# Optimization experiments

Measured on AMD Instinct MI355X. Metric: run time of the kernel, lower is better.

## Reference

```python
import jax, jax.numpy as jnp
import numpy as np
from jax.scipy.linalg import expm

B, T = 32, 4096
FREQ_DIM = 128
HID = 64
OUT_DIM = 2
N_COMP = 4
DT = 0.1
EPS = 1e-5


def setup_inputs() -> dict:
    key = jax.random.key(0)
    ks = jax.random.split(key, 16)
    f32 = jnp.float32

    def lin(k, out_d, in_d):
        bound = 1.0 / np.sqrt(in_d)
        kw, kb = jax.random.split(k)
        W = jax.random.uniform(kw, (out_d, in_d), f32, -bound, bound)
        b = jax.random.uniform(kb, (out_d,), f32, -bound, bound)
        return W, b

    x = jax.random.normal(ks[0], (B, T, 1), f32)
    # EnhancedWavePhysics params
    freq_spectrum = jnp.linspace(1.0, 20.0, FREQ_DIM, dtype=f32)
    pm_w1, pm_b1 = lin(ks[1], 128, 1)
    pm_w2, pm_b2 = lin(ks[2], FREQ_DIM * 2, 128)
    wc_w, wc_b = lin(ks[3], HID, FREQ_DIM)
    amp_ctrl = jnp.ones((1,), f32) * 0.1
    # quantum encoder
    qe_w1, qe_b1 = lin(ks[4], HID * 2, HID)
    qe_w2, qe_b2 = lin(ks[5], HID * 4, HID * 2)
    # layernorm
    ln_g = jnp.ones((HID * 4,), f32)
    ln_b = jnp.zeros((HID * 4,), f32)
    # skew-symmetric hamiltonians [4, 64, 64]
    A = jax.random.normal(ks[6], (N_COMP, HID, HID), f32) * 0.05
    hams = (A - jnp.swapaxes(A, -1, -2)) / 2.0
    # interference net
    int_w1, int_b1 = lin(ks[7], 32, 4)
    int_w2, int_b2 = lin(ks[8], OUT_DIM, 32)
    int_strength = jnp.ones((1,), f32)
    return dict(x=x, freq_spectrum=freq_spectrum, pm_w1=pm_w1, pm_b1=pm_b1,
                pm_w2=pm_w2, pm_b2=pm_b2, wc_w=wc_w, wc_b=wc_b,
                amp_ctrl=amp_ctrl, qe_w1=qe_w1, qe_b1=qe_b1, qe_w2=qe_w2,
                qe_b2=qe_b2, ln_g=ln_g, ln_b=ln_b, hams=hams,
                int_w1=int_w1, int_b1=int_b1, int_w2=int_w2, int_b2=int_b2,
                int_strength=int_strength)


def reference(x, freq_spectrum, pm_w1, pm_b1, pm_w2, pm_b2, wc_w, wc_b,
              amp_ctrl, qe_w1, qe_b1, qe_w2, qe_b2, ln_g, ln_b, hams,
              int_w1, int_b1, int_w2, int_b2, int_strength):
    Bx, Tx, _ = x.shape
    # --- EnhancedWavePhysics ---
    mod = jnp.tanh(x @ pm_w1.T + pm_b1) @ pm_w2.T + pm_b2            # [B,T,2F]
    amplitude, phase = jnp.split(mod, 2, axis=-1)                     # [B,T,F]
    amplitude = jnp.tanh(amplitude) * amp_ctrl
    time = jnp.linspace(0.0, 2.0 * np.pi, Tx)[None, :, None]          # [1,T,1]
    freqs = freq_spectrum[None, None, :]                              # [1,1,F]
    wave_components = amplitude * jnp.sin(freqs * time + phase)       # [B,T,F]
    wave_field = jnp.tanh(wave_components @ wc_w.T + wc_b)            # [B,T,H]
    # --- quantum encoder + layernorm ---
    q = jnp.tanh(wave_field @ qe_w1.T + qe_b1) @ qe_w2.T + qe_b2      # [B,T,4H]
    mu = q.mean(-1, keepdims=True)
    var = q.var(-1, keepdims=True)
    q = (q - mu) / jnp.sqrt(var + EPS) * ln_g + ln_b
    psi = q.reshape(Bx, Tx, N_COMP, HID)                              # [B,T,C,D]
    # --- Hamiltonian evolution: torch does matrix_exp(-1j*(1j*H)*dt)=expm(H*dt)
    #     (H skew-symmetric real => U real orthogonal), then psi @ U.T, take real.
    U = jax.vmap(expm)(hams * DT)                                     # [C,D,D]
    evolved = jnp.einsum('btcd,ced->btce', psi, U)                    # [B,T,C,D]
    # --- EnhancedInterference ---
    spec = jnp.abs(jnp.fft.fft(evolved, axis=1))                      # [B,T,C,D]
    freq_w = jax.nn.softmax(spec.mean(-1), axis=1)                    # [B,T,C]
    weighted = jnp.sum(spec * freq_w[..., None], axis=1)              # [B,C,D]
    spatial_avg = weighted.mean(-1)                                   # [B,C]
    out = jnp.tanh(spatial_avg @ int_w1.T + int_b1) @ int_w2.T + int_b2
    return out * int_strength                                         # [B,out_dim]
```

## Files before the change

kernel.cpp:

```cpp
#include <hip/hip_runtime.h>
#include <hip/hip_bf16.h>

#define TT 4096
#define BB 32

typedef unsigned short ushort_t;
typedef __attribute__((ext_vector_type(8))) short short8v;
typedef __attribute__((ext_vector_type(4))) float float4v;

__device__ inline ushort_t bf16rn(float v) {
    unsigned u = __float_as_uint(v);
    unsigned r = (u + 0x7FFFu + ((u >> 16) & 1u)) >> 16;
    return (ushort_t)r;
}
__device__ inline float bf16tof(ushort_t h) {
    return __uint_as_float(((unsigned)h) << 16);
}
__device__ inline int SW(int i) { return i + (i >> 5); }

__device__ inline float fast_tanh(float x) {
    float e = __builtin_amdgcn_exp2f(x * 2.8853900817779268f);
    return 1.0f - 2.0f * __builtin_amdgcn_rcpf(e + 1.0f);
}
__device__ inline float fast_sin(float x) {
    return __builtin_amdgcn_sinf(x * 0.15915494309189535f);
}

__global__ __launch_bounds__(256) void k1_expm(const float* __restrict__ hams,
                                               ushort_t* __restrict__ Uhi,
                                               ushort_t* __restrict__ Ulo)
{
    int c = blockIdx.x, tid = threadIdx.x;
    __shared__ float M[4096], P[4096], Acc[4096];
    const float* H = hams + c * 4096;
    for (int k = tid; k < 4096; k += 256) {
        float m = H[k] * 0.1f;
        M[k] = m; P[k] = m;
        Acc[k] = m + (((k >> 6) == (k & 63)) ? 1.0f : 0.0f);
    }
    __syncthreads();
    int j = tid & 63;
    float mcol[64];
    #pragma unroll
    for (int k = 0; k < 64; k++) mcol[k] = M[k * 64 + j];
    for (int term = 2; term <= 8; term++) {
        float inv = 1.0f / (float)term;
        float np_[16];
        #pragma unroll
        for (int r = 0; r < 16; r++) {
            int i = (tid >> 6) + 4 * r;
            float a = 0.f;
            #pragma unroll
            for (int k = 0; k < 64; k++) a = fmaf(P[i * 64 + k], mcol[k], a);
            np_[r] = a * inv;
        }
        __syncthreads();
        #pragma unroll
        for (int r = 0; r < 16; r++) {
            int i = (tid >> 6) + 4 * r;
            P[i * 64 + j] = np_[r];
            Acc[i * 64 + j] += np_[r];
        }
        __syncthreads();
    }
    for (int k = tid; k < 4096; k += 256) {
        float v = Acc[k];
        ushort_t h = bf16rn(v);
        Uhi[c * 4096 + k] = h;
        Ulo[c * 4096 + k] = bf16rn(v - bf16tof(h));
    }
}

__global__ void split_all(const float* __restrict__ pw2, const float* __restrict__ wcw,
                          const float* __restrict__ qw1, const float* __restrict__ qw2,
                          ushort_t* __restrict__ wb)
{
    int i = blockIdx.x * 256 + threadIdx.x;
    const float* src; ushort_t *hi, *lo; int off;
    if (i < 32768)      { src = pw2; hi = wb;          lo = wb + 32768;  off = i; }
    else if (i < 40960) { src = wcw; hi = wb + 65536;  lo = wb + 73728;  off = i - 32768; }
    else if (i < 49152) { src = qw1; hi = wb + 81920;  lo = wb + 90112;  off = i - 40960; }
    else                { src = qw2; hi = wb + 98304;  lo = wb + 131072; off = i - 49152; }
    float v = src[off];
    ushort_t h = bf16rn(v);
    hi[off] = h;
    lo[off] = bf16rn(v - bf16tof(h));
}

__global__ __launch_bounds__(256, 2) void gemm_s1(
    const ushort_t* __restrict__ Whi, const ushort_t* __restrict__ Wlo,
    const float* __restrict__ bias,
    const float* __restrict__ x, const float* __restrict__ pw1,
    const float* __restrict__ pb1,
    const float* __restrict__ freq, const float* __restrict__ ampc,
    ushort_t* __restrict__ O)
{
    __shared__ ushort_t OT[2][2048];
    int tid = threadIdx.x;
    int w = tid >> 6, l = tid & 63, l15 = l & 15, kg = l >> 4;
    int kofb = kg * 8;

    short8v bh[4][4], bl[4][4];
    #pragma unroll
    for (int i = 0; i < 4; i++) {
        int n = (w + 4 * i) * 16 + l15;
        #pragma unroll
        for (int kc = 0; kc < 4; kc++) {
            int kof = kc * 32 + kofb;
            bh[i][kc] = *(const short8v*)(Whi + (size_t)n * 128 + kof);
            bl[i][kc] = *(const short8v*)(Wlo + (size_t)n * 128 + kof);
        }
    }
    float am = ampc[0];
    float fr[2], ba[2], bp[2];
    #pragma unroll
    for (int i = 0; i < 2; i++) {
        int f = (w + 4 * i) * 16 + l15;
        fr[i] = freq[f]; ba[i] = bias[f]; bp[i] = bias[128 + f];
    }

    int mbase = blockIdx.x * 64;
    for (int mi = 0; mi < 4; mi++) {
        int m0 = mbase + mi * 16;
        float xv = x[m0 + l15];
        short8v ah[4], al[4];
        #pragma unroll
        for (int kc = 0; kc < 4; kc++) {
            int k0 = kc * 32 + kofb;
            float4 w0 = *(const float4*)(pw1 + k0);
            float4 w1v = *(const float4*)(pw1 + k0 + 4);
            float4 b0 = *(const float4*)(pb1 + k0);
            float4 b1v = *(const float4*)(pb1 + k0 + 4);
            #pragma unroll
            for (int j = 0; j < 8; j++) {
                float wj = (j < 4) ? (&w0.x)[j] : (&w1v.x)[j - 4];
                float bj = (j < 4) ? (&b0.x)[j] : (&b1v.x)[j - 4];
                float v = fast_tanh(fmaf(xv, wj, bj));
                ushort_t h = bf16rn(v);
                ah[kc][j] = (short)h;
                al[kc][j] = (short)bf16rn(v - bf16tof(h));
            }
        }
        float4v acc[4];
        #pragma unroll
        for (int i = 0; i < 4; i++) acc[i] = (float4v){0.f, 0.f, 0.f, 0.f};
        #pragma unroll
        for (int kc = 0; kc < 4; kc++) {
            #pragma unroll
            for (int i = 0; i < 4; i++) {
                acc[i] = __builtin_amdgcn_mfma_f32_16x16x32_bf16(ah[kc], bh[i][kc], acc[i], 0, 0, 0);
                acc[i] = __builtin_amdgcn_mfma_f32_16x16x32_bf16(ah[kc], bl[i][kc], acc[i], 0, 0, 0);
                acc[i] = __builtin_amdgcn_mfma_f32_16x16x32_bf16(al[kc], bh[i][kc], acc[i], 0, 0, 0);
            }
        }
        int buf = mi & 1;
        #pragma unroll
        for (int i = 0; i < 2; i++) {
            int f = (w + 4 * i) * 16 + l15;
            #pragma unroll
            for (int r = 0; r < 4; r++) {
                int m = m0 + kg * 4 + r;
                float timev = 6.283185307179586f * (float)(m & 4095) / 4095.0f;
                float a = fast_tanh(acc[i][r] + ba[i]) * am;
                float ph = acc[i + 2][r] + bp[i];
                float v = a * fast_sin(fmaf(fr[i], timev, ph));
                OT[buf][(kg * 4 + r) * 128 + f] = bf16rn(v);
            }
        }
        __syncthreads();
        *(uint4*)(O + (size_t)m0 * 128 + tid * 8) = *(const uint4*)(&OT[buf][tid * 8]);
    }
}

__global__ __launch_bounds__(256, 2) void s23_v2(
    const ushort_t* __restrict__ A,
    const ushort_t* __restrict__ W2hi, const ushort_t* __restrict__ W2lo,
    const float* __restrict__ b2,
    const ushort_t* __restrict__ W3hi, const ushort_t* __restrict__ W3lo,
    const float* __restrict__ b3,
    ushort_t* __restrict__ OHi, ushort_t* __restrict__ OLo)
{
    __shared__ unsigned WF[2][16][65];
    __shared__ ushort_t OThi[2][2048], OTlo[2][2048];
    int tid = threadIdx.x;
    int w = tid >> 6, l = tid & 63, l15 = l & 15, kg = l >> 4;
    int kofb = kg * 8;

    short8v w2h[4], w2l[4];
    #pragma unroll
    for (int kc = 0; kc < 4; kc++) {
        int n = w * 16 + l15;
        int kof = kc * 32 + kofb;
        w2h[kc] = *(const short8v*)(W2hi + (size_t)n * 128 + kof);
        w2l[kc] = *(const short8v*)(W2lo + (size_t)n * 128 + kof);
    }
    short8v w3h[2][2], w3l[2][2];
    #pragma unroll
    for (int i = 0; i < 2; i++) {
        int n = (w + 4 * i) * 16 + l15;
        #pragma unroll
        for (int kc = 0; kc < 2; kc++) {
            int kof = kc * 32 + kofb;
            w3h[i][kc] = *(const short8v*)(W3hi + (size_t)n * 64 + kof);
            w3l[i][kc] = *(const short8v*)(W3lo + (size_t)n * 64 + kof);
        }
    }
    float b2v = b2[w * 16 + l15];
    float b3v[2];
    #pragma unroll
    for (int i = 0; i < 2; i++) b3v[i] = b3[(w + 4 * i) * 16 + l15];

    int mbase = blockIdx.x * 64;
    for (int mi = 0; mi < 4; mi++) {
        int m0 = mbase + mi * 16;
        short8v ah[4];
        #pragma unroll
        for (int kc = 0; kc < 4; kc++) {
            int kof = kc * 32 + kofb;
            ah[kc] = *(const short8v*)(A + (size_t)(m0 + l15) * 128 + kof);
        }
        float4v acc1 = (float4v){0.f, 0.f, 0.f, 0.f};
        #pragma unroll
        for (int kc = 0; kc < 4; kc++) {
            acc1 = __builtin_amdgcn_mfma_f32_16x16x32_bf16(ah[kc], w2h[kc], acc1, 0, 0, 0);
            acc1 = __builtin_amdgcn_mfma_f32_16x16x32_bf16(ah[kc], w2l[kc], acc1, 0, 0, 0);
        }
        int buf = mi & 1;
        #pragma unroll
        for (int r = 0; r < 4; r++) {
            float v = fast_tanh(acc1[r] + b2v);
            ushort_t h = bf16rn(v);
            ushort_t lo2 = bf16rn(v - bf16tof(h));
            WF[buf][kg * 4 + r][w * 16 + l15] = (unsigned)h | ((unsigned)lo2 << 16);
        }
        __syncthreads();
        float4v acc2[2];
        acc2[0] = (float4v){0.f, 0.f, 0.f, 0.f};
        acc2[1] = (float4v){0.f, 0.f, 0.f, 0.f};
        #pragma unroll
        for (int kc = 0; kc < 2; kc++) {
            short8v a2h, a2l;
            #pragma unroll
            for (int j = 0; j < 8; j++) {
                unsigned u = WF[buf][l15][kc * 32 + kofb + j];
                a2h[j] = (short)(u & 0xFFFFu);
                a2l[j] = (short)(u >> 16);
            }
            #pragma unroll
            for (int i = 0; i < 2; i++) {
                acc2[i] = __builtin_amdgcn_mfma_f32_16x16x32_bf16(a2h, w3h[i][kc], acc2[i], 0, 0, 0);
                acc2[i] = __builtin_amdgcn_mfma_f32_16x16x32_bf16(a2h, w3l[i][kc], acc2[i], 0, 0, 0);
                acc2[i] = __builtin_amdgcn_mfma_f32_16x16x32_bf16(a2l, w3h[i][kc], acc2[i], 0, 0, 0);
            }
        }
        #pragma unroll
        for (int i = 0; i < 2; i++) {
            int n = (w + 4 * i) * 16 + l15;
            #pragma unroll
            for (int r = 0; r < 4; r++) {
                float v = fast_tanh(acc2[i][r] + b3v[i]);
                ushort_t h = bf16rn(v);
                OThi[buf][(kg * 4 + r) * 128 + n] = h;
                OTlo[buf][(kg * 4 + r) * 128 + n] = bf16rn(v - bf16tof(h));
            }
        }
        __syncthreads();
        *(uint4*)(OHi + (size_t)m0 * 128 + tid * 8) = *(const uint4*)(&OThi[buf][tid * 8]);
        *(uint4*)(OLo + (size_t)m0 * 128 + tid * 8) = *(const uint4*)(&OTlo[buf][tid * 8]);
    }
}

__global__ __launch_bounds__(256, 2) void gemm_s4e(
    const ushort_t* __restrict__ Ahi, const ushort_t* __restrict__ Alo,
    const ushort_t* __restrict__ Whi, const ushort_t* __restrict__ Wlo,
    const float* __restrict__ bias,
    const float* __restrict__ lng, const float* __restrict__ lnb,
    const ushort_t* __restrict__ Uhi, const ushort_t* __restrict__ Ulo,
    unsigned* __restrict__ psiu)
{
    __shared__ float partS[2][4][16], partSS[2][4][16];
    __shared__ unsigned PT[256 * 33];
    int tid = threadIdx.x;
    int w = tid >> 6, l = tid & 63, l15 = l & 15, kg = l >> 4;
    int kofb = kg * 8;

    short8v bh[4][4], bl[4][4];
    #pragma unroll
    for (int i = 0; i < 4; i++) {
        int n = (w + 4 * i) * 16 + l15;
        #pragma unroll
        for (int kc = 0; kc < 4; kc++) {
            int kof = kc * 32 + kofb;
            bh[i][kc] = *(const short8v*)(Whi + (size_t)n * 128 + kof);
            bl[i][kc] = *(const short8v*)(Wlo + (size_t)n * 128 + kof);
        }
    }
    float bv[4], g4[4], be4[4];
    #pragma unroll
    for (int i = 0; i < 4; i++) {
        int n = (w + 4 * i) * 16 + l15;
        bv[i] = bias[n]; g4[i] = lng[n]; be4[i] = lnb[n];
    }

    int mbase = blockIdx.x * 32;
    int b = mbase >> 12, tbase = mbase & 4095;

    short8v a0h[4], a0l[4], a1h[4], a1l[4];
    #pragma unroll
    for (int kc = 0; kc < 4; kc++) {
        int kof = kc * 32 + kofb;
        a0h[kc] = *(const short8v*)(Ahi + (size_t)(mbase + l15) * 128 + kof);
        a0l[kc] = *(const short8v*)(Alo + (size_t)(mbase + l15) * 128 + kof);
        a1h[kc] = *(const short8v*)(Ahi + (size_t)(mbase + 16 + l15) * 128 + kof);
        a1l[kc] = *(const short8v*)(Alo + (size_t)(mbase + 16 + l15) * 128 + kof);
    }

    float4v acc0[4], acc1[4];
    #pragma unroll
    for (int i = 0; i < 4; i++) {
        acc0[i] = (float4v){0.f, 0.f, 0.f, 0.f};
        acc1[i] = (float4v){0.f, 0.f, 0.f, 0.f};
    }
    #pragma unroll
    for (int kc = 0; kc < 4; kc++) {
        #pragma unroll
        for (int i = 0; i < 4; i++) {
            acc0[i] = __builtin_amdgcn_mfma_f32_16x16x32_bf16(a0h[kc], bh[i][kc], acc0[i], 0, 0, 0);
            acc0[i] = __builtin_amdgcn_mfma_f32_16x16x32_bf16(a0h[kc], bl[i][kc], acc0[i], 0, 0, 0);
            acc0[i] = __builtin_amdgcn_mfma_f32_16x16x32_bf16(a0l[kc], bh[i][kc], acc0[i], 0, 0, 0);
        }
    }
    #pragma unroll
    for (int kc = 0; kc < 4; kc++) {
        #pragma unroll
        for (int i = 0; i < 4; i++) {
            acc1[i] = __builtin_amdgcn_mfma_f32_16x16x32_bf16(a1h[kc], bh[i][kc], acc1[i], 0, 0, 0);
            acc1[i] = __builtin_amdgcn_mfma_f32_16x16x32_bf16(a1h[kc], bl[i][kc], acc1[i], 0, 0, 0);
            acc1[i] = __builtin_amdgcn_mfma_f32_16x16x32_bf16(a1l[kc], bh[i][kc], acc1[i], 0, 0, 0);
        }
    }

    #pragma unroll
    for (int mi = 0; mi < 2; mi++) {
        float4v* acc = (mi == 0) ? acc0 : acc1;
        float s[4] = {0, 0, 0, 0}, ss[4] = {0, 0, 0, 0};
        #pragma unroll
        for (int i = 0; i < 4; i++) {
            #pragma unroll
            for (int r = 0; r < 4; r++) {
                float v = acc[i][r] + bv[i];
                s[r] += v; ss[r] += v * v;
            }
        }
        #pragma unroll
        for (int r = 0; r < 4; r++) {
            #pragma unroll
            for (int off = 1; off < 16; off <<= 1) {
                s[r] += __shfl_xor(s[r], off);
                ss[r] += __shfl_xor(ss[r], off);
            }
        }
        if (l15 == 0) {
            #pragma unroll
            for (int r = 0; r < 4; r++) {
                partS[mi][w][kg * 4 + r] = s[r];
                partSS[mi][w][kg * 4 + r] = ss[r];
            }
        }
    }
    __syncthreads();

    #pragma unroll
    for (int mi = 0; mi < 2; mi++) {
        float4v* acc = (mi == 0) ? acc0 : acc1;
        float mu[4], rstd[4];
        #pragma unroll
        for (int r = 0; r < 4; r++) {
            float ts = 0.f, tss = 0.f;
            #pragma unroll
            for (int wv = 0; wv < 4; wv++) {
                ts += partS[mi][wv][kg * 4 + r];
                tss += partSS[mi][wv][kg * 4 + r];
            }
            mu[r] = ts * (1.0f / 256.0f);
            float var = tss * (1.0f / 256.0f) - mu[r] * mu[r];
            rstd[r] = rsqrtf(var + 1e-5f);
        }
        #pragma unroll
        for (int i = 0; i < 4; i++) {
            int n = (w + 4 * i) * 16 + l15;
            #pragma unroll
            for (int r = 0; r < 4; r++) {
                float v = (acc[i][r] + bv[i] - mu[r]) * rstd[r] * g4[i] + be4[i];
                ushort_t h = bf16rn(v);
                ushort_t lo2 = bf16rn(v - bf16tof(h));
                PT[n * 33 + mi * 16 + kg * 4 + r] = (unsigned)h | ((unsigned)lo2 << 16);
            }
        }
    }
    __syncthreads();

    int c = w;
    size_t gb = ((size_t)(b * 256 + c * 64)) * 4096 + tbase;
    #pragma unroll
    for (int et = 0; et < 4; et++) {
        short8v ua_h[2], ua_l[2];
        #pragma unroll
        for (int kc = 0; kc < 2; kc++) {
            size_t uo = (size_t)c * 4096 + (et * 16 + l15) * 64 + kc * 32 + kofb;
            ua_h[kc] = *(const short8v*)(Uhi + uo);
            ua_l[kc] = *(const short8v*)(Ulo + uo);
        }
        #pragma unroll
        for (int tt = 0; tt < 2; tt++) {
            float4v acc = (float4v){0.f, 0.f, 0.f, 0.f};
            #pragma unroll
            for (int kc = 0; kc < 2; kc++) {
                short8v b_h, b_l;
                #pragma unroll
                for (int j = 0; j < 8; j++) {
                    unsigned u = PT[(c * 64 + kc * 32 + kofb + j) * 33 + tt * 16 + l15];
                    b_h[j] = (short)(u & 0xFFFFu);
                    b_l[j] = (short)(u >> 16);
                }
                acc = __builtin_amdgcn_mfma_f32_16x16x32_bf16(ua_h[kc], b_h, acc, 0, 0, 0);
                acc = __builtin_amdgcn_mfma_f32_16x16x32_bf16(ua_h[kc], b_l, acc, 0, 0, 0);
                acc = __builtin_amdgcn_mfma_f32_16x16x32_bf16(ua_l[kc], b_h, acc, 0, 0, 0);
            }
            #pragma unroll
            for (int r = 0; r < 4; r++) {
                int e = et * 16 + kg * 4 + r;
                float v = acc[r];
                ushort_t h = bf16rn(v);
                ushort_t lo2 = bf16rn(v - bf16tof(h));
                psiu[gb + (size_t)e * 4096 + tt * 16 + l15] =
                    (unsigned)h | ((unsigned)lo2 << 16);
            }
        }
    }
}

__global__ __launch_bounds__(256, 2) void k3b_fft(const unsigned* __restrict__ ev,
                                                  float* __restrict__ msum8)
{
    __shared__ float re[4224], im[4224];
    int b = blockIdx.x, c = blockIdx.y, g = blockIdx.z;
    int tid = threadIdx.x;

    float macc[8];
    #pragma unroll
    for (int r = 0; r < 8; r++) macc[r] = 0.f;
    float macc8 = 0.f;

    size_t base = (((size_t)b * 4 + c) * 64 + (size_t)g * 8) * TT;
    for (int p = 0; p < 4; p++) {
        __syncthreads();
        for (int r = 0; r < 4; r++) {
            int t0 = (r * 256 + tid) * 4;
            uint4 va = *(const uint4*)(ev + base + (size_t)(2 * p) * TT + t0);
            uint4 vb = *(const uint4*)(ev + base + (size_t)(2 * p + 1) * TT + t0);
            #pragma unroll
            for (int j = 0; j < 4; j++) {
                int rv = __brev((unsigned)(t0 + j)) >> 20;
                unsigned ua = (&va.x)[j], ub = (&vb.x)[j];
                re[SW(rv)] = bf16tof((ushort_t)(ua & 0xFFFFu)) + bf16tof((ushort_t)(ua >> 16));
                im[SW(rv)] = bf16tof((ushort_t)(ub & 0xFFFFu)) + bf16tof((ushort_t)(ub >> 16));
            }
        }
        __syncthreads();

        #pragma unroll
        for (int trip = 0; trip < 3; trip++) {
            const int sh = trip * 4;
            int pos = tid & ((1 << sh) - 1);
            int grp = tid >> sh;
            int i0 = (grp << (sh + 4)) + pos;

            float yr[16], yi[16];
            #pragma unroll
            for (int j = 0; j < 16; j++) {
                int a = SW(i0 + (j << sh));
                yr[j] = re[a]; yi[j] = im[a];
            }
            float ang = -(float)pos / (float)(16 << sh);
            float t1r = __builtin_amdgcn_cosf(ang);
            float t1i = __builtin_amdgcn_sinf(ang);
            float t2r = t1r * t1r - t1i * t1i, t2i = 2.f * t1r * t1i;
            float t4r = t2r * t2r - t2i * t2i, t4i = 2.f * t2r * t2i;
            float t8r = t4r * t4r - t4i * t4i, t8i = 2.f * t4r * t4i;

            #pragma unroll
            for (int m = 0; m < 8; m++) {
                int j0 = 2 * m, j1 = j0 + 1;
                float tr = t8r * yr[j1] - t8i * yi[j1];
                float ti = t8r * yi[j1] + t8i * yr[j1];
                yr[j1] = yr[j0] - tr; yi[j1] = yi[j0] - ti;
                yr[j0] += tr;         yi[j0] += ti;
            }
            #pragma unroll
            for (int bs = 0; bs < 16; bs += 4) {
                {
                    int j0 = bs, j1 = bs + 2;
                    float tr = t4r * yr[j1] - t4i * yi[j1];
                    float ti = t4r * yi[j1] + t4i * yr[j1];
                    yr[j1] = yr[j0] - tr; yi[j1] = yi[j0] - ti;
                    yr[j0] += tr;         yi[j0] += ti;
                }
                {
                    int j0 = bs + 1, j1 = bs + 3;
                    float tr = t4i * yr[j1] + t4r * yi[j1];
                    float ti = t4i * yi[j1] - t4r * yr[j1];
                    yr[j1] = yr[j0] - tr; yi[j1] = yi[j0] - ti;
                    yr[j0] += tr;         yi[j0] += ti;
                }
            }
            {
                float wr = t2r, wi = t2i;
                #pragma unroll
                for (int j = 0; j < 4; j++) {
                    #pragma unroll
                    for (int bs = 0; bs < 16; bs += 8) {
                        int j0 = bs + j, j1 = j0 + 4;
                        float tr = wr * yr[j1] - wi * yi[j1];
                        float ti = wr * yi[j1] + wi * yr[j1];
                        yr[j1] = yr[j0] - tr; yi[j1] = yi[j0] - ti;
                        yr[j0] += tr;         yi[j0] += ti;
                    }
                    float nwr = (wr + wi) * 0.70710678f;
                    float nwi = (wi - wr) * 0.70710678f;
                    wr = nwr; wi = nwi;
                }
            }
            {
                float wr = t1r, wi = t1i;
                #pragma unroll
                for (int j = 0; j < 8; j++) {
                    int j0 = j, j1 = j + 8;
                    float tr = wr * yr[j1] - wi * yi[j1];
                    float ti = wr * yi[j1] + wi * yr[j1];
                    yr[j1] = yr[j0] - tr; yi[j1] = yi[j0] - ti;
                    yr[j0] += tr;         yi[j0] += ti;
                    float nwr = wr * 0.92387953f + wi * 0.38268343f;
                    float nwi = wi * 0.92387953f - wr * 0.38268343f;
                    wr = nwr; wi = nwi;
                }
            }
            #pragma unroll
            for (int j = 0; j < 16; j++) {
                int a = SW(i0 + (j << sh));
                re[a] = yr[j]; im[a] = yi[j];
            }
            __syncthreads();
        }

        for (int r = 0; r < 8; r++) {
            int k = tid + r * 256;
            int mk = (4096 - k) & 4095;
            float rk = re[SW(k)], ik = im[SW(k)];
            float rm = re[SW(mk)], imm = im[SW(mk)];
            float dA1 = rk + rm, dA2 = ik - imm;
            float dB1 = ik + imm, dB2 = rk - rm;
            float magA = 0.5f * sqrtf(dA1 * dA1 + dA2 * dA2);
            float magB = 0.5f * sqrtf(dB1 * dB1 + dB2 * dB2);
            macc[r] += magA + magB;
        }
        if (tid == 0) {
            float rk = re[SW(2048)], ik = im[SW(2048)];
            macc8 += fabsf(rk) + fabsf(ik);
        }
    }
    float* ms = msum8 + (((size_t)b * 4 + c) * 8 + g) * 4096;
    for (int r = 0; r < 8; r++) {
        int k = tid + r * 256;
        ms[k] = macc[r];
        if (k > 0) ms[4096 - k] = macc[r];
    }
    if (tid == 0) ms[2048] = macc8;
}

__global__ __launch_bounds__(256) void k4_softdot(const float* __restrict__ msum8,
                                                  float* __restrict__ sa)
{
    __shared__ float m[4096];
    __shared__ float red[256];
    int bc = blockIdx.x, tid = threadIdx.x;
    const float* ms = msum8 + (size_t)bc * 8 * 4096;
    float lmax = -1e30f;
    for (int k = tid; k < 4096; k += 256) {
        float v = 0.f;
        #pragma unroll
        for (int g = 0; g < 8; g++) v += ms[g * 4096 + k];
        v *= (1.0f / 64.0f);
        m[k] = v;
        lmax = fmaxf(lmax, v);
    }
    red[tid] = lmax; __syncthreads();
    for (int s2 = 128; s2 > 0; s2 >>= 1) {
        if (tid < s2) red[tid] = fmaxf(red[tid], red[tid + s2]);
        __syncthreads();
    }
    float mx = red[0]; __syncthreads();
    float lsum = 0.f, ldot = 0.f;
    for (int k = tid; k < 4096; k += 256) {
        float e = expf(m[k] - mx);
        lsum += e; ldot += e * m[k];
    }
    red[tid] = lsum; __syncthreads();
    for (int s2 = 128; s2 > 0; s2 >>= 1) {
        if (tid < s2) red[tid] += red[tid + s2];
        __syncthreads();
    }
    float tsum = red[0]; __syncthreads();
    red[tid] = ldot; __syncthreads();
    for (int s2 = 128; s2 > 0; s2 >>= 1) {
        if (tid < s2) red[tid] += red[tid + s2];
        __syncthreads();
    }
    if (tid == 0) sa[bc] = red[0] / tsum;
}

__global__ void k5_head(const float* __restrict__ sa,
                        const float* __restrict__ w1, const float* __restrict__ b1,
                        const float* __restrict__ w2, const float* __restrict__ b2,
                        const float* __restrict__ strength,
                        float* __restrict__ out)
{
    int b = threadIdx.x;
    if (b >= 32) return;
    float s0 = sa[b * 4 + 0], s1 = sa[b * 4 + 1];
    float s2 = sa[b * 4 + 2], s3 = sa[b * 4 + 3];
    float h[32];
    #pragma unroll
    for (int j = 0; j < 32; j++)
        h[j] = tanhf(b1[j] + w1[j * 4 + 0] * s0 + w1[j * 4 + 1] * s1 +
                     w1[j * 4 + 2] * s2 + w1[j * 4 + 3] * s3);
    float st = strength[0];
    #pragma unroll
    for (int o = 0; o < 2; o++) {
        float a = b2[o];
        #pragma unroll
        for (int j = 0; j < 32; j++) a = fmaf(w2[o * 32 + j], h[j], a);
        out[b * 2 + o] = a * st;
    }
}

extern "C" void kernel_launch(void* const* d_in, const int* in_sizes, int n_in,
                              void* d_out, int out_size, void* d_ws, size_t ws_size,
                              hipStream_t stream)
{
    const float* x    = (const float*)d_in[0];
    const float* freq = (const float*)d_in[1];
    const float* pw1  = (const float*)d_in[2];
    const float* pb1  = (const float*)d_in[3];
    const float* pw2  = (const float*)d_in[4];
    const float* pb2  = (const float*)d_in[5];
    const float* wcw  = (const float*)d_in[6];
    const float* wcb  = (const float*)d_in[7];
    const float* ampc = (const float*)d_in[8];
    const float* qw1  = (const float*)d_in[9];
    const float* qb1  = (const float*)d_in[10];
    const float* qw2  = (const float*)d_in[11];
    const float* qb2  = (const float*)d_in[12];
    const float* lng  = (const float*)d_in[13];
    const float* lnb  = (const float*)d_in[14];
    const float* hams = (const float*)d_in[15];
    const float* iw1  = (const float*)d_in[16];
    const float* ib1  = (const float*)d_in[17];
    const float* iw2  = (const float*)d_in[18];
    const float* ib2  = (const float*)d_in[19];
    const float* istr = (const float*)d_in[20];

    char* wsb = (char*)d_ws;
    ushort_t* AHi = (ushort_t*)(wsb + 0);
    ushort_t* ALo = (ushort_t*)(wsb + 33554432);
    ushort_t* Bwcf = (ushort_t*)(wsb + 67108864);
    unsigned* psi = (unsigned*)(wsb + 67108864);
    float*    msum8 = (float*)(wsb + 0);
    ushort_t* Uhi  = (ushort_t*)(wsb + 201326592);
    ushort_t* Ulo  = (ushort_t*)(wsb + 201359360);
    float*    sa   = (float*)(wsb + 201392128);
    ushort_t* wb   = (ushort_t*)(wsb + 203489792);
    ushort_t *pw2hi = wb,          *pw2lo = wb + 32768;
    ushort_t *wcwhi = wb + 65536,  *wcwlo = wb + 73728;
    ushort_t *qw1hi = wb + 81920,  *qw1lo = wb + 90112;
    ushort_t *qw2hi = wb + 98304,  *qw2lo = wb + 131072;
    float* out = (float*)d_out;

    k1_expm<<<4, 256, 0, stream>>>(hams, Uhi, Ulo);
    split_all<<<320, 256, 0, stream>>>(pw2, wcw, qw1, qw2, wb);

    gemm_s1<<<2048, 256, 0, stream>>>(pw2hi, pw2lo, pb2, x, pw1, pb1,
                                      freq, ampc, Bwcf);
    s23_v2<<<2048, 256, 0, stream>>>(Bwcf, wcwhi, wcwlo, wcb,
        qw1hi, qw1lo, qb1, AHi, ALo);
    gemm_s4e<<<4096, 256, 0, stream>>>(AHi, ALo, qw2hi, qw2lo, qb2,
        lng, lnb, Uhi, Ulo, psi);

    k3b_fft<<<dim3(32, 4, 8), 256, 0, stream>>>(psi, msum8);
    k4_softdot<<<128, 256, 0, stream>>>(msum8, sa);
    k5_head<<<1, 64, 0, stream>>>(sa, iw1, ib1, iw2, ib2, istr, out);
}
```

Baseline: 381.8 us.

## Fuse wave-compress, encoder layers and layernorm into one kernel

Merges the s23 kernel (wave-compress GEMM plus first encoder layer) with the second encoder GEMM, layernorm and Hamiltonian kernel into a single kernel. The hi/lo split intermediate no longer goes to global memory and is passed through shared memory instead. The qw2 weight fragments are now loaded from global (cached) memory inside the loop rather than held in registers, which saves registers but adds repeated loads. The FFT magnitude also switches to the hardware sqrt intrinsic.

```diff
diff --git a/kernel.cpp b/kernel.cpp
--- a/kernel.cpp
+++ b/kernel.cpp
@@ -172,16 +172,22 @@
     }
 }
 
-__global__ __launch_bounds__(256, 2) void s23_v2(
+__global__ __launch_bounds__(256, 2) void gemm_s234e(
     const ushort_t* __restrict__ A,
     const ushort_t* __restrict__ W2hi, const ushort_t* __restrict__ W2lo,
     const float* __restrict__ b2,
     const ushort_t* __restrict__ W3hi, const ushort_t* __restrict__ W3lo,
     const float* __restrict__ b3,
-    ushort_t* __restrict__ OHi, ushort_t* __restrict__ OLo)
+    const ushort_t* __restrict__ W4hi, const ushort_t* __restrict__ W4lo,
+    const float* __restrict__ b4,
+    const float* __restrict__ lng, const float* __restrict__ lnb,
+    const ushort_t* __restrict__ Uhi, const ushort_t* __restrict__ Ulo,
+    unsigned* __restrict__ psiu)
 {
     __shared__ unsigned WF[2][16][65];
-    __shared__ ushort_t OThi[2][2048], OTlo[2][2048];
+    __shared__ unsigned Q1[2][16][132];
+    __shared__ float partS[2][4][16], partSS[2][4][16];
+    __shared__ unsigned PT[256 * 33];
     int tid = threadIdx.x;
     int w = tid >> 6, l = tid & 63, l15 = l & 15, kg = l >> 4;
     int kofb = kg * 8;
@@ -209,9 +215,25 @@
     float b3v[2];
     #pragma unroll
     for (int i = 0; i < 2; i++) b3v[i] = b3[(w + 4 * i) * 16 + l15];
-
-    int mbase = blockIdx.x * 64;
-    for (int mi = 0; mi < 4; mi++) {
+    float bv[4], g4[4], be4[4];
+    #pragma unroll
+    for (int i = 0; i < 4; i++) {
+        int n = (w + 4 * i) * 16 + l15;
+        bv[i] = b4[n]; g4[i] = lng[n]; be4[i] = lnb[n];
+    }
+
+    int mbase = blockIdx.x * 32;
+    int b = mbase >> 12, tbase = mbase & 4095;
+
+    float4v acc0[4], acc1[4];
+    #pragma unroll
+    for (int i = 0; i < 4; i++) {
+        acc0[i] = (float4v){0.f, 0.f, 0.f, 0.f};
+        acc1[i] = (float4v){0.f, 0.f, 0.f, 0.f};
+    }
+
+    #pragma unroll
+    for (int mi = 0; mi < 2; mi++) {
         int m0 = mbase + mi * 16;
         short8v ah[4];
         #pragma unroll
@@ -219,38 +241,37 @@
             int kof = kc * 32 + kofb;
             ah[kc] = *(const short8v*)(A + (size_t)(m0 + l15) * 128 + kof);
         }
-        float4v acc1 = (float4v){0.f, 0.f, 0.f, 0.f};
+        float4v acw = (float4v){0.f, 0.f, 0.f, 0.f};
         #pragma unroll
         for (int kc = 0; kc < 4; kc++) {
-            acc1 = __builtin_amdgcn_mfma_f32_16x16x32_bf16(ah[kc], w2h[kc], acc1, 0, 0, 0);
-            acc1 = __builtin_amdgcn_mfma_f32_16x16x32_bf16(ah[kc], w2l[kc], acc1, 0, 0, 0);
-        }
-        int buf = mi & 1;
+            acw = __builtin_amdgcn_mfma_f32_16x16x32_bf16(ah[kc], w2h[kc], acw, 0, 0, 0);
+            acw = __builtin_amdgcn_mfma_f32_16x16x32_bf16(ah[kc], w2l[kc], acw, 0, 0, 0);
+        }
         #pragma unroll
         for (int r = 0; r < 4; r++) {
-            float v = fast_tanh(acc1[r] + b2v);
+            float v = fast_tanh(acw[r] + b2v);
             ushort_t h = bf16rn(v);
             ushort_t lo2 = bf16rn(v - bf16tof(h));
-            WF[buf][kg * 4 + r][w * 16 + l15] = (unsigned)h | ((unsigned)lo2 << 16);
-        }
-        __syncthreads();
-        float4v acc2[2];
-        acc2[0] = (float4v){0.f, 0.f, 0.f, 0.f};
-        acc2[1] = (float4v){0.f, 0.f, 0.f, 0.f};
+            WF[mi][kg * 4 + r][w * 16 + l15] = (unsigned)h | ((unsigned)lo2 << 16);
+        }
+        __syncthreads();
+        float4v acq[2];
+        acq[0] = (float4v){0.f, 0.f, 0.f, 0.f};
+        acq[1] = (float4v){0.f, 0.f, 0.f, 0.f};
         #pragma unroll
         for (int kc = 0; kc < 2; kc++) {
             short8v a2h, a2l;
             #pragma unroll
             for (int j = 0; j < 8; j++) {
-                unsigned u = WF[buf][l15][kc * 32 + kofb + j];
+                unsigned u = WF[mi][l15][kc * 32 + kofb + j];
                 a2h[j] = (short)(u & 0xFFFFu);
                 a2l[j] = (short)(u >> 16);
             }
             #pragma unroll
             for (int i = 0; i < 2; i++) {
-                acc2[i] = __builtin_amdgcn_mfma_f32_16x16x32_bf16(a2h, w3h[i][kc], acc2[i], 0, 0, 0);
-                acc2[i] = __builtin_amdgcn_mfma_f32_16x16x32_bf16(a2h, w3l[i][kc], acc2[i], 0, 0, 0);
-                acc2[i] = __builtin_amdgcn_mfma_f32_16x16x32_bf16(a2l, w3h[i][kc], acc2[i], 0, 0, 0);
+                acq[i] = __builtin_amdgcn_mfma_f32_16x16x32_bf16(a2h, w3h[i][kc], acq[i], 0, 0, 0);
+                acq[i] = __builtin_amdgcn_mfma_f32_16x16x32_bf16(a2h, w3l[i][kc], acq[i], 0, 0, 0);
+                acq[i] = __builtin_amdgcn_mfma_f32_16x16x32_bf16(a2l, w3h[i][kc], acq[i], 0, 0, 0);
             }
         }
         #pragma unroll
@@ -258,91 +279,37 @@
             int n = (w + 4 * i) * 16 + l15;
             #pragma unroll
             for (int r = 0; r < 4; r++) {
-                float v = fast_tanh(acc2[i][r] + b3v[i]);
+                float v = fast_tanh(acq[i][r] + b3v[i]);
                 ushort_t h = bf16rn(v);
-                OThi[buf][(kg * 4 + r) * 128 + n] = h;
-                OTlo[buf][(kg * 4 + r) * 128 + n] = bf16rn(v - bf16tof(h));
-            }
-        }
-        __syncthreads();
-        *(uint4*)(OHi + (size_t)m0 * 128 + tid * 8) = *(const uint4*)(&OThi[buf][tid * 8]);
-        *(uint4*)(OLo + (size_t)m0 * 128 + tid * 8) = *(const uint4*)(&OTlo[buf][tid * 8]);
-    }
-}
-
-__global__ __launch_bounds__(256, 2) void gemm_s4e(
-    const ushort_t* __restrict__ Ahi, const ushort_t* __restrict__ Alo,
-    const ushort_t* __restrict__ Whi, const ushort_t* __restrict__ Wlo,
-    const float* __restrict__ bias,
-    const float* __restrict__ lng, const float* __restrict__ lnb,
-    const ushort_t* __restrict__ Uhi, const ushort_t* __restrict__ Ulo,
-    unsigned* __restrict__ psiu)
-{
-    __shared__ float partS[2][4][16], partSS[2][4][16];
-    __shared__ unsigned PT[256 * 33];
-    int tid = threadIdx.x;
-    int w = tid >> 6, l = tid & 63, l15 = l & 15, kg = l >> 4;
-    int kofb = kg * 8;
-
-    short8v bh[4][4], bl[4][4];
-    #pragma unroll
-    for (int i = 0; i < 4; i++) {
-        int n = (w + 4 * i) * 16 + l15;
+                ushort_t lo2 = bf16rn(v - bf16tof(h));
+                Q1[mi][kg * 4 + r][n] = (unsigned)h | ((unsigned)lo2 << 16);
+            }
+        }
+        __syncthreads();
+        short8v a4h[4], a4l[4];
+        #pragma unroll
+        for (int kc = 0; kc < 4; kc++) {
+            #pragma unroll
+            for (int j = 0; j < 8; j++) {
+                unsigned u = Q1[mi][l15][kc * 32 + kofb + j];
+                a4h[kc][j] = (short)(u & 0xFFFFu);
+                a4l[kc][j] = (short)(u >> 16);
+            }
+        }
+        float4v* acc = (mi == 0) ? acc0 : acc1;
         #pragma unroll
         for (int kc = 0; kc < 4; kc++) {
             int kof = kc * 32 + kofb;
-            bh[i][kc] = *(const short8v*)(Whi + (size_t)n * 128 + kof);
-            bl[i][kc] = *(const short8v*)(Wlo + (size_t)n * 128 + kof);
-        }
-    }
-    float bv[4], g4[4], be4[4];
-    #pragma unroll
-    for (int i = 0; i < 4; i++) {
-        int n = (w + 4 * i) * 16 + l15;
-        bv[i] = bias[n]; g4[i] = lng[n]; be4[i] = lnb[n];
-    }
-
-    int mbase = blockIdx.x * 32;
-    int b = mbase >> 12, tbase = mbase & 4095;
-
-    short8v a0h[4], a0l[4], a1h[4], a1l[4];
-    #pragma unroll
-    for (int kc = 0; kc < 4; kc++) {
-        int kof = kc * 32 + kofb;
-        a0h[kc] = *(const short8v*)(Ahi + (size_t)(mbase + l15) * 128 + kof);
-        a0l[kc] = *(const short8v*)(Alo + (size_t)(mbase + l15) * 128 + kof);
-        a1h[kc] = *(const short8v*)(Ahi + (size_t)(mbase + 16 + l15) * 128 + kof);
-        a1l[kc] = *(const short8v*)(Alo + (size_t)(mbase + 16 + l15) * 128 + kof);
-    }
-
-    float4v acc0[4], acc1[4];
-    #pragma unroll
-    for (int i = 0; i < 4; i++) {
-        acc0[i] = (float4v){0.f, 0.f, 0.f, 0.f};
-        acc1[i] = (float4v){0.f, 0.f, 0.f, 0.f};
-    }
-    #pragma unroll
-    for (int kc = 0; kc < 4; kc++) {
-        #pragma unroll
-        for (int i = 0; i < 4; i++) {
-            acc0[i] = __builtin_amdgcn_mfma_f32_16x16x32_bf16(a0h[kc], bh[i][kc], acc0[i], 0, 0, 0);
-            acc0[i] = __builtin_amdgcn_mfma_f32_16x16x32_bf16(a0h[kc], bl[i][kc], acc0[i], 0, 0, 0);
-            acc0[i] = __builtin_amdgcn_mfma_f32_16x16x32_bf16(a0l[kc], bh[i][kc], acc0[i], 0, 0, 0);
-        }
-    }
-    #pragma unroll
-    for (int kc = 0; kc < 4; kc++) {
-        #pragma unroll
-        for (int i = 0; i < 4; i++) {
-            acc1[i] = __builtin_amdgcn_mfma_f32_16x16x32_bf16(a1h[kc], bh[i][kc], acc1[i], 0, 0, 0);
-            acc1[i] = __builtin_amdgcn_mfma_f32_16x16x32_bf16(a1h[kc], bl[i][kc], acc1[i], 0, 0, 0);
-            acc1[i] = __builtin_amdgcn_mfma_f32_16x16x32_bf16(a1l[kc], bh[i][kc], acc1[i], 0, 0, 0);
-        }
-    }
-
-    #pragma unroll
-    for (int mi = 0; mi < 2; mi++) {
-        float4v* acc = (mi == 0) ? acc0 : acc1;
+            #pragma unroll
+            for (int i = 0; i < 4; i++) {
+                int n = (w + 4 * i) * 16 + l15;
+                short8v qbh = *(const short8v*)(W4hi + (size_t)n * 128 + kof);
+                short8v qbl = *(const short8v*)(W4lo + (size_t)n * 128 + kof);
+                acc[i] = __builtin_amdgcn_mfma_f32_16x16x32_bf16(a4h[kc], qbh, acc[i], 0, 0, 0);
+                acc[i] = __builtin_amdgcn_mfma_f32_16x16x32_bf16(a4h[kc], qbl, acc[i], 0, 0, 0);
+                acc[i] = __builtin_amdgcn_mfma_f32_16x16x32_bf16(a4l[kc], qbh, acc[i], 0, 0, 0);
+            }
+        }
         float s[4] = {0, 0, 0, 0}, ss[4] = {0, 0, 0, 0};
         #pragma unroll
         for (int i = 0; i < 4; i++) {
@@ -560,8 +527,8 @@
             float rm = re[SW(mk)], imm = im[SW(mk)];
             float dA1 = rk + rm, dA2 = ik - imm;
             float dB1 = ik + imm, dB2 = rk - rm;
-            float magA = 0.5f * sqrtf(dA1 * dA1 + dA2 * dA2);
-            float magB = 0.5f * sqrtf(dB1 * dB1 + dB2 * dB2);
+            float magA = 0.5f * __builtin_amdgcn_sqrtf(dA1 * dA1 + dA2 * dA2);
+            float magB = 0.5f * __builtin_amdgcn_sqrtf(dB1 * dB1 + dB2 * dB2);
             macc[r] += magA + magB;
         }
         if (tid == 0) {
@@ -671,11 +638,9 @@
     const float* istr = (const float*)d_in[20];
 
     char* wsb = (char*)d_ws;
-    ushort_t* AHi = (ushort_t*)(wsb + 0);
-    ushort_t* ALo = (ushort_t*)(wsb + 33554432);
-    ushort_t* Bwcf = (ushort_t*)(wsb + 67108864);
+    ushort_t* Bwcf = (ushort_t*)(wsb + 0);
+    float*    msum8 = (float*)(wsb + 0);
     unsigned* psi = (unsigned*)(wsb + 67108864);
-    float*    msum8 = (float*)(wsb + 0);
     ushort_t* Uhi  = (ushort_t*)(wsb + 201326592);
     ushort_t* Ulo  = (ushort_t*)(wsb + 201359360);
     float*    sa   = (float*)(wsb + 201392128);
@@ -691,10 +656,8 @@
 
     gemm_s1<<<2048, 256, 0, stream>>>(pw2hi, pw2lo, pb2, x, pw1, pb1,
                                       freq, ampc, Bwcf);
-    s23_v2<<<2048, 256, 0, stream>>>(Bwcf, wcwhi, wcwlo, wcb,
-        qw1hi, qw1lo, qb1, AHi, ALo);
-    gemm_s4e<<<4096, 256, 0, stream>>>(AHi, ALo, qw2hi, qw2lo, qb2,
-        lng, lnb, Uhi, Ulo, psi);
+    gemm_s234e<<<4096, 256, 0, stream>>>(Bwcf, wcwhi, wcwlo, wcb,
+        qw1hi, qw1lo, qb1, qw2hi, qw2lo, qb2, lng, lnb, Uhi, Ulo, psi);
 
     k3b_fft<<<dim3(32, 4, 8), 256, 0, stream>>>(psi, msum8);
     k4_softdot<<<128, 256, 0, stream>>>(msum8, sa);
```

After: 413.4 us. 1.08x slower.
